# Kernel tuning notes

Measured on AMD Instinct MI355X. Metric: run time of the kernel, lower is better.

The kernel has to match this reference:

```python
import jax, jax.numpy as jnp
import numpy as np

CELL = 128
STEPS = 20
N_KEYS = 4   # ['first_conn','second_conn','first_op','second_op']
N_OUT = 6


def setup_inputs() -> dict:
    key = jax.random.key(0)
    ks = jax.random.split(key, 10)
    s = 0.05
    return {
        "net": jax.random.randint(ks[0], (STEPS,), 0, N_OUT),          # sampled actions, each in [0,6)
        "reward": jax.random.uniform(ks[1], (1,), dtype=jnp.float32),   # unused in forward (kept for signature parity)
        "emb_start": jax.random.normal(ks[2], (1, CELL), jnp.float32) * s,          # Embedding(1,128)
        "emb_keys": jax.random.normal(ks[3], (N_KEYS, N_OUT, CELL), jnp.float32) * s,
        "fc_W": jax.random.normal(ks[4], (N_KEYS, N_OUT, CELL), jnp.float32) * s,
        "fc_b": jax.random.normal(ks[5], (N_KEYS, N_OUT), jnp.float32) * s,
        "W_ih": jax.random.normal(ks[6], (4 * CELL, CELL), jnp.float32) * s,  # LSTMCell input weights (i,f,g,o)
        "W_hh": jax.random.normal(ks[7], (4 * CELL, CELL), jnp.float32) * s,  # LSTMCell hidden weights
        "b_ih": jax.random.normal(ks[8], (4 * CELL,), jnp.float32) * s,
        "b_hh": jax.random.normal(ks[9], (4 * CELL,), jnp.float32) * s,
    }


def _lstm_cell(x, h, c, W_ih, W_hh, b_ih, b_hh):
    # PyTorch LSTMCell: gates ordered (i, f, g, o)
    gates = x @ W_ih.T + b_ih + h @ W_hh.T + b_hh   # [1, 4*CELL]
    i, f, g, o = jnp.split(gates, 4, axis=-1)
    c_new = jax.nn.sigmoid(f) * c + jax.nn.sigmoid(i) * jnp.tanh(g)
    h_new = jax.nn.sigmoid(o) * jnp.tanh(c_new)
    return h_new, c_new


def reference(net, reward, emb_start, emb_keys, fc_W, fc_b, W_ih, W_hh, b_ih, b_hh):
    key_idx = jnp.arange(STEPS) % N_KEYS            # which head/embedding at each step
    fc_W_t = fc_W[key_idx]                          # [STEPS, 6, CELL]
    fc_b_t = fc_b[key_idx]                          # [STEPS, 6]
    emb_t = emb_keys[key_idx, net]                  # [STEPS, CELL] next-step input embedding

    def step(carry, xs):
        h, c, x = carry
        Wt, bt, ev = xs
        h, c = _lstm_cell(x, h, c, W_ih, W_hh, b_ih, b_hh)
        probs = jax.nn.softmax(h @ Wt.T + bt, axis=1)   # [1, 6]
        return (h, c, ev[None, :]), probs

    h0 = jnp.zeros((1, CELL), dtype=emb_start.dtype)
    c0 = jnp.zeros((1, CELL), dtype=emb_start.dtype)
    x0 = emb_start                                   # embedding lookup of action 0 in a 1-row table
    _, outputs = jax.lax.scan(step, (h0, c0, x0), (fc_W_t, fc_b_t, emb_t))
    return outputs                                   # [STEPS, 1, 6], stacked version of the torch list
```

## Files before the change

### kernel.cpp

```cpp
#include <hip/hip_runtime.h>
#include <hip/hip_fp16.h>

#define CELL 128
#define STEPS 20

typedef _Float16 half8_t __attribute__((ext_vector_type(8)));
typedef float    floatx4 __attribute__((ext_vector_type(4)));

__device__ __forceinline__ unsigned packf2(float x, float y) {
    typedef _Float16 h2 __attribute__((ext_vector_type(2)));
    h2 h = { (_Float16)x, (_Float16)y };
    return __builtin_bit_cast(unsigned, h);
}
__device__ __forceinline__ float fdot2u(unsigned a, unsigned b, float c) {
    typedef _Float16 h2 __attribute__((ext_vector_type(2)));
#if __has_builtin(__builtin_amdgcn_fdot2)
    return __builtin_amdgcn_fdot2(__builtin_bit_cast(h2, a), __builtin_bit_cast(h2, b), c, false);
#else
    h2 x = __builtin_bit_cast(h2, a), y = __builtin_bit_cast(h2, b);
    return fmaf((float)x[0], (float)y[0], fmaf((float)x[1], (float)y[1], c));
#endif
}
__device__ __forceinline__ float fast_sigmoid(float x) { return 1.0f / (1.0f + __expf(-x)); }
__device__ __forceinline__ float fast_tanh(float x) {
    return 2.0f / (1.0f + __expf(-2.0f * x)) - 1.0f;
}


__global__ void __launch_bounds__(256)
nas_conv_kernel(const float* __restrict__ W_ih, const float* __restrict__ W_hh,
                const float* __restrict__ b_ih, const float* __restrict__ b_hh,
                uint4* __restrict__ wsf, float* __restrict__ wsb)
{
    const int tid = blockIdx.x * 256 + threadIdx.x;
    for (int f = tid; f < 16384; f += 8192) {
        const int t0 = f >> 5, rem = f & 31, kc = rem >> 2, tau = rem & 3;
        const int wv = t0 >> 6, lane = t0 & 63, quad = lane >> 4, lcol = lane & 15;
        const int r  = (wv << 6) + (tau << 4) + lcol;
        const int k0 = (kc << 5) + (quad << 3);
        const float* src = (k0 < CELL) ? (W_ih + r * CELL + k0)
                                       : (W_hh + r * CELL + (k0 - CELL));
        float4 a = ((const float4*)src)[0], b = ((const float4*)src)[1];
        half8_t h = { (_Float16)a.x, (_Float16)a.y, (_Float16)a.z, (_Float16)a.w,
                      (_Float16)b.x, (_Float16)b.y, (_Float16)b.z, (_Float16)b.w };
        wsf[f] = __builtin_bit_cast(uint4, h);
    }
    if (tid < 512) wsb[tid] = b_ih[tid] + b_hh[tid];
}

extern "C" __global__ void __launch_bounds__(512, 1)
nas_policy_kernel(const int* __restrict__ net,
                  const float* __restrict__ emb_start,
                  const float* __restrict__ emb_keys,
                  const float* __restrict__ fc_W,
                  const float* __restrict__ fc_b,
                  const uint4* __restrict__ wsf,
                  const float* __restrict__ wsb,
                  float* __restrict__ out)
{
    const int t0   = threadIdx.x;
    const int wv   = t0 >> 6;
    const int lane = t0 & 63;
    const int lcol = lane & 15;

    __shared__ __align__(16) unsigned xh2[2 * 64];
    __shared__ __align__(16) unsigned hp2[2 * 64];
    __shared__ __align__(16) unsigned s_embk2[24 * 64];
    __shared__ unsigned s_fcw2[24 * 64];
    __shared__ float gates[4 * CELL];
    __shared__ float s_fcb[24];
    __shared__ float logits[2 * 8];
    __shared__ int   s_net[STEPS];

    const uint4* wf = wsf + t0 * 32;
    half8_t bf0[8], bf1[8], bf2[8], bf3[8];
#pragma unroll
    for (int kc = 0; kc < 8; ++kc) {
        bf0[kc] = __builtin_bit_cast(half8_t, wf[kc * 4 + 0]);
        bf1[kc] = __builtin_bit_cast(half8_t, wf[kc * 4 + 1]);
        bf2[kc] = __builtin_bit_cast(half8_t, wf[kc * 4 + 2]);
        bf3[kc] = __builtin_bit_cast(half8_t, wf[kc * 4 + 3]);
    }
    const int rb = (wv << 6) + lcol;
    const float bias0 = wsb[rb], bias1 = wsb[rb + 16], bias2 = wsb[rb + 32], bias3 = wsb[rb + 48];

    {
        const float2* ek2 = (const float2*)emb_keys;
        const float2* fw2 = (const float2*)fc_W;
        for (int i = t0; i < 24 * 64; i += 512) {
            float2 v = ek2[i]; s_embk2[i] = packf2(v.x, v.y);
            float2 w = fw2[i]; s_fcw2[i]  = packf2(w.x, w.y);
        }
        if (t0 < 24)    s_fcb[t0] = fc_b[t0];
        if (t0 < STEPS) s_net[t0] = net[t0];
        if (t0 < 64) {
            float2 v = ((const float2*)emb_start)[t0];
            xh2[t0]      = packf2(v.x, v.y);
            xh2[64 + t0] = 0u;
        }
    }
    float c = 0.0f;
    const int rbase = wv << 6;

    for (int t = 0; t < STEPS; ++t) {
        __syncthreads();

        floatx4 acc0 = {0,0,0,0}, acc1 = {0,0,0,0}, acc2 = {0,0,0,0}, acc3 = {0,0,0,0};
        const uint4* xp = (const uint4*)xh2;
        const int quad = lane >> 4;
#pragma unroll
        for (int kc = 0; kc < 8; ++kc) {
            uint4 u = xp[(kc << 2) + quad];
            half8_t af = __builtin_bit_cast(half8_t, u);
            acc0 = __builtin_amdgcn_mfma_f32_16x16x32_f16(af, bf0[kc], acc0, 0, 0, 0);
            acc1 = __builtin_amdgcn_mfma_f32_16x16x32_f16(af, bf1[kc], acc1, 0, 0, 0);
            acc2 = __builtin_amdgcn_mfma_f32_16x16x32_f16(af, bf2[kc], acc2, 0, 0, 0);
            acc3 = __builtin_amdgcn_mfma_f32_16x16x32_f16(af, bf3[kc], acc3, 0, 0, 0);
        }
        if (lane < 16) {
            gates[rbase + lane]      = acc0[0] + bias0;
            gates[rbase + 16 + lane] = acc1[0] + bias1;
            gates[rbase + 32 + lane] = acc2[0] + bias2;
            gates[rbase + 48 + lane] = acc3[0] + bias3;
        }

        if (t >= 2 && wv == 5 && lane < 6) {
            const float* L = logits + ((t & 1) << 3);
            float l0 = L[0], l1 = L[1], l2 = L[2], l3 = L[3], l4 = L[4], l5 = L[5];
            float m = fmaxf(fmaxf(fmaxf(l0, l1), fmaxf(l2, l3)), fmaxf(l4, l5));
            float e0 = __expf(l0 - m), e1 = __expf(l1 - m), e2 = __expf(l2 - m);
            float e3 = __expf(l3 - m), e4 = __expf(l4 - m), e5 = __expf(l5 - m);
            float s = ((e0 + e1) + (e2 + e3)) + (e4 + e5);
            float mine = (lane == 0) ? e0 : (lane == 1) ? e1 : (lane == 2) ? e2
                       : (lane == 3) ? e3 : (lane == 4) ? e4 : e5;
            out[(t - 2) * 6 + lane] = mine / s;
        }

        __syncthreads();

        if (t0 < CELL) {
            float ig = fast_sigmoid(gates[t0]);
            float fg = fast_sigmoid(gates[CELL + t0]);
            float gg = fast_tanh   (gates[2 * CELL + t0]);
            float og = fast_sigmoid(gates[3 * CELL + t0]);
            c = fg * c + ig * gg;
            float h = og * fast_tanh(c);
            float hpv = __shfl_xor(h, 1);
            if ((t0 & 1) == 0) {
                unsigned u = packf2(h, hpv);
                xh2[64 + (t0 >> 1)] = u;
                hp2[((t & 1) << 6) + (t0 >> 1)] = u;
            }
        }
        if (wv == 2 && t < STEPS - 1) {
            xh2[lane] = s_embk2[((((t + 1) & 3) * 6) + s_net[t + 1]) * 64 + lane];
        }
        if (t >= 1 && wv >= 2) {
            const int ti = t - 1, hd = wv - 2;
            unsigned hu = hp2[((ti & 1) << 6) + lane];
            unsigned wu = s_fcw2[(((ti & 3) * 6) + hd) * 64 + lane];
            float p = fdot2u(hu, wu, 0.0f);
#pragma unroll
            for (int off = 32; off >= 1; off >>= 1) p += __shfl_down(p, off);
            if (lane == 0)
                logits[((ti & 1) << 3) + hd] = p + s_fcb[(ti & 3) * 6 + hd];
        }
    }

    __syncthreads();
    if (wv >= 2) {
        const int hd = wv - 2;
        unsigned hu = hp2[(1 << 6) + lane];
        unsigned wu = s_fcw2[(((19 & 3) * 6) + hd) * 64 + lane];
        float p = fdot2u(hu, wu, 0.0f);
#pragma unroll
        for (int off = 32; off >= 1; off >>= 1) p += __shfl_down(p, off);
        if (lane == 0) logits[(1 << 3) + hd] = p + s_fcb[(19 & 3) * 6 + hd];
    }
    if (wv == 0 && lane < 6) {
        const float* L = logits + 0;
        float l0 = L[0], l1 = L[1], l2 = L[2], l3 = L[3], l4 = L[4], l5 = L[5];
        float m = fmaxf(fmaxf(fmaxf(l0, l1), fmaxf(l2, l3)), fmaxf(l4, l5));
        float e0 = __expf(l0 - m), e1 = __expf(l1 - m), e2 = __expf(l2 - m);
        float e3 = __expf(l3 - m), e4 = __expf(l4 - m), e5 = __expf(l5 - m);
        float s = ((e0 + e1) + (e2 + e3)) + (e4 + e5);
        float mine = (lane == 0) ? e0 : (lane == 1) ? e1 : (lane == 2) ? e2
                   : (lane == 3) ? e3 : (lane == 4) ? e4 : e5;
        out[18 * 6 + lane] = mine / s;
    }
    __syncthreads();
    if (wv == 0 && lane < 6) {
        const float* L = logits + 8;
        float l0 = L[0], l1 = L[1], l2 = L[2], l3 = L[3], l4 = L[4], l5 = L[5];
        float m = fmaxf(fmaxf(fmaxf(l0, l1), fmaxf(l2, l3)), fmaxf(l4, l5));
        float e0 = __expf(l0 - m), e1 = __expf(l1 - m), e2 = __expf(l2 - m);
        float e3 = __expf(l3 - m), e4 = __expf(l4 - m), e5 = __expf(l5 - m);
        float s = ((e0 + e1) + (e2 + e3)) + (e4 + e5);
        float mine = (lane == 0) ? e0 : (lane == 1) ? e1 : (lane == 2) ? e2
                   : (lane == 3) ? e3 : (lane == 4) ? e4 : e5;
        out[19 * 6 + lane] = mine / s;
    }
}

extern "C" __global__ void __launch_bounds__(512, 1)
nas_policy_fb(const int* __restrict__ net, const float* __restrict__ emb_start,
              const float* __restrict__ emb_keys, const float* __restrict__ fc_W,
              const float* __restrict__ fc_b, const float* __restrict__ W_ih,
              const float* __restrict__ W_hh, const float* __restrict__ b_ih,
              const float* __restrict__ b_hh, float* __restrict__ out)
{
    const int t0 = threadIdx.x, wv = t0 >> 6, lane = t0 & 63;
    const int quad = lane >> 4, lcol = lane & 15;
    __shared__ __align__(16) unsigned xh2[2 * 64];
    __shared__ __align__(16) unsigned s_embk2[24 * 64];
    __shared__ float gates[4 * CELL];
    __shared__ float s_fcW[24 * CELL];
    __shared__ float s_fcb[24];
    __shared__ float logits[2 * 8];
    __shared__ int   s_net[STEPS];
    const int rbase = wv << 6;
    const int r0 = rbase + lcol, r1 = r0 + 16, r2 = r0 + 32, r3 = r0 + 48;
    half8_t bf0[8], bf1[8], bf2[8], bf3[8];
#pragma unroll
    for (int kc = 0; kc < 8; ++kc) {
        const int k0 = (kc << 5) + (quad << 3);
        const float* base = (k0 < 128) ? W_ih + k0 : W_hh + (k0 - 128);
#define LD8(dst, row) { const float4* p4 = (const float4*)(base + (row) * CELL); \
        float4 a = p4[0], b = p4[1]; \
        dst = half8_t{ (_Float16)a.x, (_Float16)a.y, (_Float16)a.z, (_Float16)a.w, \
                       (_Float16)b.x, (_Float16)b.y, (_Float16)b.z, (_Float16)b.w }; }
        LD8(bf0[kc], r0) LD8(bf1[kc], r1) LD8(bf2[kc], r2) LD8(bf3[kc], r3)
#undef LD8
    }
    const float bias0 = b_ih[r0] + b_hh[r0], bias1 = b_ih[r1] + b_hh[r1];
    const float bias2 = b_ih[r2] + b_hh[r2], bias3 = b_ih[r3] + b_hh[r3];
    {
        const float2* ek2 = (const float2*)emb_keys;
        for (int i = t0; i < 24 * 64; i += 512) { float2 v = ek2[i]; s_embk2[i] = packf2(v.x, v.y); }
        for (int i = t0; i < 24 * CELL; i += 512) s_fcW[i] = fc_W[i];
        if (t0 < 24) s_fcb[t0] = fc_b[t0];
        if (t0 < STEPS) s_net[t0] = net[t0];
        if (t0 < 64) { float2 v = ((const float2*)emb_start)[t0];
                       xh2[t0] = packf2(v.x, v.y); xh2[64 + t0] = 0u; }
    }
    float c = 0.0f;
    for (int t = 0; t < STEPS; ++t) {
        __syncthreads();
        floatx4 a0 = {0,0,0,0}, a1 = {0,0,0,0}, a2 = {0,0,0,0}, a3 = {0,0,0,0};
        const uint4* xp = (const uint4*)xh2;
#pragma unroll
        for (int kc = 0; kc < 8; ++kc) {
            half8_t af = __builtin_bit_cast(half8_t, xp[(kc << 2) + quad]);
            a0 = __builtin_amdgcn_mfma_f32_16x16x32_f16(af, bf0[kc], a0, 0, 0, 0);
            a1 = __builtin_amdgcn_mfma_f32_16x16x32_f16(af, bf1[kc], a1, 0, 0, 0);
            a2 = __builtin_amdgcn_mfma_f32_16x16x32_f16(af, bf2[kc], a2, 0, 0, 0);
            a3 = __builtin_amdgcn_mfma_f32_16x16x32_f16(af, bf3[kc], a3, 0, 0, 0);
        }
        if (lane < 16) {
            gates[rbase + lane]      = a0[0] + bias0;
            gates[rbase + 16 + lane] = a1[0] + bias1;
            gates[rbase + 32 + lane] = a2[0] + bias2;
            gates[rbase + 48 + lane] = a3[0] + bias3;
        }
        if (t >= 1 && wv < 6) {
            const int ti = t - 1;
            unsigned hu = xh2[64 + lane];
            const float* Wr = s_fcW + (((ti & 3) * 6) + wv) * CELL;
            typedef _Float16 h2t __attribute__((ext_vector_type(2)));
            h2t hh = __builtin_bit_cast(h2t, hu);
            float p2 = (float)hh[0] * Wr[2 * lane] + (float)hh[1] * Wr[2 * lane + 1];
#pragma unroll
            for (int off = 32; off >= 1; off >>= 1) p2 += __shfl_down(p2, off);
            if (lane == 0) logits[((ti & 1) << 3) + wv] = p2 + s_fcb[(ti & 3) * 6 + wv];
        }
        if (t >= 2 && t0 < 6) {
            const float* L = logits + ((t & 1) << 3);
            float l0 = L[0], l1 = L[1], l2 = L[2], l3 = L[3], l4 = L[4], l5 = L[5];
            float m = fmaxf(fmaxf(fmaxf(l0, l1), fmaxf(l2, l3)), fmaxf(l4, l5));
            float e0 = __expf(l0 - m), e1 = __expf(l1 - m), e2 = __expf(l2 - m);
            float e3 = __expf(l3 - m), e4 = __expf(l4 - m), e5 = __expf(l5 - m);
            float s = ((e0 + e1) + (e2 + e3)) + (e4 + e5);
            float mine = (t0 == 0) ? e0 : (t0 == 1) ? e1 : (t0 == 2) ? e2
                       : (t0 == 3) ? e3 : (t0 == 4) ? e4 : e5;
            out[(t - 2) * 6 + t0] = mine / s;
        }
        __syncthreads();
        if (t0 < CELL) {
            float ig = fast_sigmoid(gates[t0]);
            float fg = fast_sigmoid(gates[CELL + t0]);
            float gg = fast_tanh(gates[2 * CELL + t0]);
            float og = fast_sigmoid(gates[3 * CELL + t0]);
            c = fg * c + ig * gg;
            float h = og * fast_tanh(c);
            float hpv = __shfl_xor(h, 1);
            if ((t0 & 1) == 0) xh2[64 + (t0 >> 1)] = packf2(h, hpv);
        } else if (wv == 2 && t < STEPS - 1) {
            xh2[lane] = s_embk2[((((t + 1) & 3) * 6) + s_net[t + 1]) * 64 + lane];
        }
    }
    __syncthreads();
    if (wv < 6) {
        unsigned hu = xh2[64 + lane];
        const float* Wr = s_fcW + (((19 & 3) * 6) + wv) * CELL;
        typedef _Float16 h2t __attribute__((ext_vector_type(2)));
        h2t hh = __builtin_bit_cast(h2t, hu);
        float p2 = (float)hh[0] * Wr[2 * lane] + (float)hh[1] * Wr[2 * lane + 1];
#pragma unroll
        for (int off = 32; off >= 1; off >>= 1) p2 += __shfl_down(p2, off);
        if (lane == 0) logits[8 + wv] = p2 + s_fcb[(19 & 3) * 6 + wv];
    }
    if (t0 < 6) {
        const float* L = logits + 0;
        float l0 = L[0], l1 = L[1], l2 = L[2], l3 = L[3], l4 = L[4], l5 = L[5];
        float m = fmaxf(fmaxf(fmaxf(l0, l1), fmaxf(l2, l3)), fmaxf(l4, l5));
        float e0 = __expf(l0 - m), e1 = __expf(l1 - m), e2 = __expf(l2 - m);
        float e3 = __expf(l3 - m), e4 = __expf(l4 - m), e5 = __expf(l5 - m);
        float s = ((e0 + e1) + (e2 + e3)) + (e4 + e5);
        float mine = (t0 == 0) ? e0 : (t0 == 1) ? e1 : (t0 == 2) ? e2
                   : (t0 == 3) ? e3 : (t0 == 4) ? e4 : e5;
        out[18 * 6 + t0] = mine / s;
    }
    __syncthreads();
    if (t0 < 6) {
        const float* L = logits + 8;
        float l0 = L[0], l1 = L[1], l2 = L[2], l3 = L[3], l4 = L[4], l5 = L[5];
        float m = fmaxf(fmaxf(fmaxf(l0, l1), fmaxf(l2, l3)), fmaxf(l4, l5));
        float e0 = __expf(l0 - m), e1 = __expf(l1 - m), e2 = __expf(l2 - m);
        float e3 = __expf(l3 - m), e4 = __expf(l4 - m), e5 = __expf(l5 - m);
        float s = ((e0 + e1) + (e2 + e3)) + (e4 + e5);
        float mine = (t0 == 0) ? e0 : (t0 == 1) ? e1 : (t0 == 2) ? e2
                   : (t0 == 3) ? e3 : (t0 == 4) ? e4 : e5;
        out[19 * 6 + t0] = mine / s;
    }
}

extern "C" void kernel_launch(void* const* d_in, const int* in_sizes, int n_in,
                              void* d_out, int out_size, void* d_ws, size_t ws_size,
                              hipStream_t stream) {
    (void)in_sizes; (void)n_in; (void)out_size;
    const int*   net       = (const int*)d_in[0];
    const float* emb_start = (const float*)d_in[2];
    const float* emb_keys  = (const float*)d_in[3];
    const float* fc_W      = (const float*)d_in[4];
    const float* fc_b      = (const float*)d_in[5];
    const float* W_ih      = (const float*)d_in[6];
    const float* W_hh      = (const float*)d_in[7];
    const float* b_ih      = (const float*)d_in[8];
    const float* b_hh      = (const float*)d_in[9];
    float*       out       = (float*)d_out;

    if (ws_size >= (size_t)(262144 + 2048)) {
        uint4* wsf = (uint4*)d_ws;
        float* wsb = (float*)((char*)d_ws + 262144);
        hipLaunchKernelGGL(nas_conv_kernel, dim3(32), dim3(256), 0, stream,
                           W_ih, W_hh, b_ih, b_hh, wsf, wsb);
        hipLaunchKernelGGL(nas_policy_kernel, dim3(1), dim3(512), 0, stream,
                           net, emb_start, emb_keys, fc_W, fc_b, wsf, wsb, out);
    } else {
        hipLaunchKernelGGL(nas_policy_fb, dim3(1), dim3(512), 0, stream,
                           net, emb_start, emb_keys, fc_W, fc_b,
                           W_ih, W_hh, b_ih, b_hh, out);
    }
}
```

Measured before the change: 103.8 us.

## Precompute input-gate projections for all steps and run recurrence on hidden-only MFMAs

The conv kernel now computes W_ih·x + biases for every step up front in fp32. This is possible because the inputs are fixed embeddings chosen by net and do not depend on the recurrence. The policy kernel loads these into shared memory, so each step only needs the W_hh·h MFMAs (half the K). Gate layout is reorganised so each wave's lanes hold the i/f/g/o outputs for the same hidden units directly, removing the gates shared buffer and one barrier per step. Softmax is deferred to a single parallel pass at the end. In exchange it adds a 40KB shared buffer and a heavier pre-kernel, and it changes the fallback kernel's embedding index, which looks like an unrelated bug fix.

```diff
diff --git a/kernel.cpp b/kernel.cpp
--- a/kernel.cpp
+++ b/kernel.cpp
@@ -30,175 +30,150 @@
 __global__ void __launch_bounds__(256)
 nas_conv_kernel(const float* __restrict__ W_ih, const float* __restrict__ W_hh,
                 const float* __restrict__ b_ih, const float* __restrict__ b_hh,
-                uint4* __restrict__ wsf, float* __restrict__ wsb)
+                const float* __restrict__ emb_start, const float* __restrict__ emb_keys,
+                const int* __restrict__ net,
+                uint4* __restrict__ wsf, float* __restrict__ wsg)
 {
     const int tid = blockIdx.x * 256 + threadIdx.x;
-    for (int f = tid; f < 16384; f += 8192) {
-        const int t0 = f >> 5, rem = f & 31, kc = rem >> 2, tau = rem & 3;
+    {
+        const int f = tid;
+        const int t0 = f >> 4, rem = f & 15, kc = rem >> 2, tau = rem & 3;
         const int wv = t0 >> 6, lane = t0 & 63, quad = lane >> 4, lcol = lane & 15;
-        const int r  = (wv << 6) + (tau << 4) + lcol;
-        const int k0 = (kc << 5) + (quad << 3);
-        const float* src = (k0 < CELL) ? (W_ih + r * CELL + k0)
-                                       : (W_hh + r * CELL + (k0 - CELL));
-        float4 a = ((const float4*)src)[0], b = ((const float4*)src)[1];
+        const int r  = tau * 128 + wv * 16 + lcol;
+        const int k0 = kc * 32 + quad * 8;
+        const float4* s4 = (const float4*)(W_hh + r * CELL + k0);
+        float4 a = s4[0], b = s4[1];
         half8_t h = { (_Float16)a.x, (_Float16)a.y, (_Float16)a.z, (_Float16)a.w,
                       (_Float16)b.x, (_Float16)b.y, (_Float16)b.z, (_Float16)b.w };
         wsf[f] = __builtin_bit_cast(uint4, h);
     }
-    if (tid < 512) wsb[tid] = b_ih[tid] + b_hh[tid];
+    for (int f = tid; f < STEPS * 512; f += 8192) {
+        const int t = f >> 9, r = f & 511;
+        const float* x = (t == 0) ? emb_start
+                       : emb_keys + ((((t - 1) & 3) * 6) + net[t - 1]) * CELL;
+        const float4* xr = (const float4*)x;
+        const float4* wr = (const float4*)(W_ih + r * CELL);
+        float a0 = 0.f, a1 = 0.f, a2 = 0.f, a3 = 0.f;
+#pragma unroll
+        for (int q = 0; q < 32; ++q) {
+            float4 w = wr[q], v = xr[q];
+            a0 = fmaf(w.x, v.x, a0); a1 = fmaf(w.y, v.y, a1);
+            a2 = fmaf(w.z, v.z, a2); a3 = fmaf(w.w, v.w, a3);
+        }
+        wsg[f] = (a0 + a1) + (a2 + a3) + b_ih[r] + b_hh[r];
+    }
 }
 
 extern "C" __global__ void __launch_bounds__(512, 1)
-nas_policy_kernel(const int* __restrict__ net,
-                  const float* __restrict__ emb_start,
-                  const float* __restrict__ emb_keys,
-                  const float* __restrict__ fc_W,
+nas_policy_kernel(const float* __restrict__ fc_W,
                   const float* __restrict__ fc_b,
                   const uint4* __restrict__ wsf,
-                  const float* __restrict__ wsb,
+                  const float* __restrict__ wsg,
                   float* __restrict__ out)
 {
     const int t0   = threadIdx.x;
     const int wv   = t0 >> 6;
     const int lane = t0 & 63;
-    const int lcol = lane & 15;
-
-    __shared__ __align__(16) unsigned xh2[2 * 64];
-    __shared__ __align__(16) unsigned hp2[2 * 64];
-    __shared__ __align__(16) unsigned s_embk2[24 * 64];
+    const int quad = lane >> 4;
+
+    __shared__ __align__(16) unsigned hbuf[2 * 64];
+    __shared__ __align__(16) float    s_gx[STEPS * 512];
     __shared__ unsigned s_fcw2[24 * 64];
-    __shared__ float gates[4 * CELL];
-    __shared__ float s_fcb[24];
-    __shared__ float logits[2 * 8];
-    __shared__ int   s_net[STEPS];
-
-    const uint4* wf = wsf + t0 * 32;
-    half8_t bf0[8], bf1[8], bf2[8], bf3[8];
-#pragma unroll
-    for (int kc = 0; kc < 8; ++kc) {
+    __shared__ float    s_fcb[24];
+    __shared__ float    llog[STEPS * 8];
+
+    const uint4* wf = wsf + t0 * 16;
+    half8_t bf0[4], bf1[4], bf2[4], bf3[4];
+#pragma unroll
+    for (int kc = 0; kc < 4; ++kc) {
         bf0[kc] = __builtin_bit_cast(half8_t, wf[kc * 4 + 0]);
         bf1[kc] = __builtin_bit_cast(half8_t, wf[kc * 4 + 1]);
         bf2[kc] = __builtin_bit_cast(half8_t, wf[kc * 4 + 2]);
         bf3[kc] = __builtin_bit_cast(half8_t, wf[kc * 4 + 3]);
     }
-    const int rb = (wv << 6) + lcol;
-    const float bias0 = wsb[rb], bias1 = wsb[rb + 16], bias2 = wsb[rb + 32], bias3 = wsb[rb + 48];
 
     {
-        const float2* ek2 = (const float2*)emb_keys;
+        const float4* g4 = (const float4*)wsg;
+        float4* sg4 = (float4*)s_gx;
+        for (int i = t0; i < STEPS * 128; i += 512) sg4[i] = g4[i];
         const float2* fw2 = (const float2*)fc_W;
-        for (int i = t0; i < 24 * 64; i += 512) {
-            float2 v = ek2[i]; s_embk2[i] = packf2(v.x, v.y);
-            float2 w = fw2[i]; s_fcw2[i]  = packf2(w.x, w.y);
-        }
-        if (t0 < 24)    s_fcb[t0] = fc_b[t0];
-        if (t0 < STEPS) s_net[t0] = net[t0];
-        if (t0 < 64) {
-            float2 v = ((const float2*)emb_start)[t0];
-            xh2[t0]      = packf2(v.x, v.y);
-            xh2[64 + t0] = 0u;
-        }
+        for (int i = t0; i < 24 * 64; i += 512) { float2 w = fw2[i]; s_fcw2[i] = packf2(w.x, w.y); }
+        if (t0 < 24) s_fcb[t0] = fc_b[t0];
+        if (t0 < 64) hbuf[64 + t0] = 0u;
     }
     float c = 0.0f;
-    const int rbase = wv << 6;
+    __syncthreads();
 
     for (int t = 0; t < STEPS; ++t) {
-        __syncthreads();
-
-        floatx4 acc0 = {0,0,0,0}, acc1 = {0,0,0,0}, acc2 = {0,0,0,0}, acc3 = {0,0,0,0};
-        const uint4* xp = (const uint4*)xh2;
-        const int quad = lane >> 4;
-#pragma unroll
-        for (int kc = 0; kc < 8; ++kc) {
-            uint4 u = xp[(kc << 2) + quad];
+        const uint4* hp4 = (const uint4*)(hbuf + (((t + 1) & 1) << 6));
+        floatx4 a0 = {0,0,0,0}, a1 = {0,0,0,0}, a2 = {0,0,0,0}, a3 = {0,0,0,0};
+#pragma unroll
+        for (int kc = 0; kc < 4; ++kc) {
+            uint4 u = hp4[(kc << 2) + quad];
             half8_t af = __builtin_bit_cast(half8_t, u);
-            acc0 = __builtin_amdgcn_mfma_f32_16x16x32_f16(af, bf0[kc], acc0, 0, 0, 0);
-            acc1 = __builtin_amdgcn_mfma_f32_16x16x32_f16(af, bf1[kc], acc1, 0, 0, 0);
-            acc2 = __builtin_amdgcn_mfma_f32_16x16x32_f16(af, bf2[kc], acc2, 0, 0, 0);
-            acc3 = __builtin_amdgcn_mfma_f32_16x16x32_f16(af, bf3[kc], acc3, 0, 0, 0);
-        }
+            a0 = __builtin_amdgcn_mfma_f32_16x16x32_f16(af, bf0[kc], a0, 0, 0, 0);
+            a1 = __builtin_amdgcn_mfma_f32_16x16x32_f16(af, bf1[kc], a1, 0, 0, 0);
+            a2 = __builtin_amdgcn_mfma_f32_16x16x32_f16(af, bf2[kc], a2, 0, 0, 0);
+            a3 = __builtin_amdgcn_mfma_f32_16x16x32_f16(af, bf3[kc], a3, 0, 0, 0);
+        }
+
+        if (t >= 1 && wv >= 6 && lane >= 16) {
+            const int hd = (wv - 6) * 3 + (lane >> 4) - 1;
+            const int li = lane & 15;
+            const int hg = ((t - 1) & 3) * 6 + hd;
+            const unsigned* hb = hbuf + (((t + 1) & 1) << 6);
+            const unsigned* wp = s_fcw2 + hg * 64 + li * 4;
+            float p = fdot2u(hb[li * 4],     wp[0], 0.0f);
+            p = fdot2u(hb[li * 4 + 1], wp[1], p);
+            p = fdot2u(hb[li * 4 + 2], wp[2], p);
+            p = fdot2u(hb[li * 4 + 3], wp[3], p);
+            p += __shfl_down(p, 8); p += __shfl_down(p, 4);
+            p += __shfl_down(p, 2); p += __shfl_down(p, 1);
+            if (li == 0) llog[(t - 1) * 8 + hd] = p + s_fcb[hg];
+        }
+
         if (lane < 16) {
-            gates[rbase + lane]      = acc0[0] + bias0;
-            gates[rbase + 16 + lane] = acc1[0] + bias1;
-            gates[rbase + 32 + lane] = acc2[0] + bias2;
-            gates[rbase + 48 + lane] = acc3[0] + bias3;
-        }
-
-        if (t >= 2 && wv == 5 && lane < 6) {
-            const float* L = logits + ((t & 1) << 3);
-            float l0 = L[0], l1 = L[1], l2 = L[2], l3 = L[3], l4 = L[4], l5 = L[5];
-            float m = fmaxf(fmaxf(fmaxf(l0, l1), fmaxf(l2, l3)), fmaxf(l4, l5));
-            float e0 = __expf(l0 - m), e1 = __expf(l1 - m), e2 = __expf(l2 - m);
-            float e3 = __expf(l3 - m), e4 = __expf(l4 - m), e5 = __expf(l5 - m);
-            float s = ((e0 + e1) + (e2 + e3)) + (e4 + e5);
-            float mine = (lane == 0) ? e0 : (lane == 1) ? e1 : (lane == 2) ? e2
-                       : (lane == 3) ? e3 : (lane == 4) ? e4 : e5;
-            out[(t - 2) * 6 + lane] = mine / s;
-        }
-
-        __syncthreads();
-
-        if (t0 < CELL) {
-            float ig = fast_sigmoid(gates[t0]);
-            float fg = fast_sigmoid(gates[CELL + t0]);
-            float gg = fast_tanh   (gates[2 * CELL + t0]);
-            float og = fast_sigmoid(gates[3 * CELL + t0]);
+            const int base = t * 512 + (wv << 4) + lane;
+            float ig = fast_sigmoid(a0[0] + s_gx[base]);
+            float fg = fast_sigmoid(a1[0] + s_gx[base + 128]);
+            float gg = fast_tanh   (a2[0] + s_gx[base + 256]);
+            float og = fast_sigmoid(a3[0] + s_gx[base + 384]);
             c = fg * c + ig * gg;
             float h = og * fast_tanh(c);
             float hpv = __shfl_xor(h, 1);
-            if ((t0 & 1) == 0) {
-                unsigned u = packf2(h, hpv);
-                xh2[64 + (t0 >> 1)] = u;
-                hp2[((t & 1) << 6) + (t0 >> 1)] = u;
-            }
-        }
-        if (wv == 2 && t < STEPS - 1) {
-            xh2[lane] = s_embk2[((((t + 1) & 3) * 6) + s_net[t + 1]) * 64 + lane];
-        }
-        if (t >= 1 && wv >= 2) {
-            const int ti = t - 1, hd = wv - 2;
-            unsigned hu = hp2[((ti & 1) << 6) + lane];
-            unsigned wu = s_fcw2[(((ti & 3) * 6) + hd) * 64 + lane];
-            float p = fdot2u(hu, wu, 0.0f);
-#pragma unroll
-            for (int off = 32; off >= 1; off >>= 1) p += __shfl_down(p, off);
-            if (lane == 0)
-                logits[((ti & 1) << 3) + hd] = p + s_fcb[(ti & 3) * 6 + hd];
-        }
-    }
-
+            if ((lane & 1) == 0)
+                hbuf[((t & 1) << 6) + (wv << 3) + (lane >> 1)] = packf2(h, hpv);
+        }
+
+        __syncthreads();
+    }
+
+    if (wv >= 6 && lane >= 16) {
+        const int hd = (wv - 6) * 3 + (lane >> 4) - 1;
+        const int li = lane & 15;
+        const int hg = (19 & 3) * 6 + hd;
+        const unsigned* hb = hbuf + 64;
+        const unsigned* wp = s_fcw2 + hg * 64 + li * 4;
+        float p = fdot2u(hb[li * 4],     wp[0], 0.0f);
+        p = fdot2u(hb[li * 4 + 1], wp[1], p);
+        p = fdot2u(hb[li * 4 + 2], wp[2], p);
+        p = fdot2u(hb[li * 4 + 3], wp[3], p);
+        p += __shfl_down(p, 8); p += __shfl_down(p, 4);
+        p += __shfl_down(p, 2); p += __shfl_down(p, 1);
+        if (li == 0) llog[19 * 8 + hd] = p + s_fcb[hg];
+    }
     __syncthreads();
-    if (wv >= 2) {
-        const int hd = wv - 2;
-        unsigned hu = hp2[(1 << 6) + lane];
-        unsigned wu = s_fcw2[(((19 & 3) * 6) + hd) * 64 + lane];
-        float p = fdot2u(hu, wu, 0.0f);
-#pragma unroll
-        for (int off = 32; off >= 1; off >>= 1) p += __shfl_down(p, off);
-        if (lane == 0) logits[(1 << 3) + hd] = p + s_fcb[(19 & 3) * 6 + hd];
-    }
-    if (wv == 0 && lane < 6) {
-        const float* L = logits + 0;
+    if (t0 < STEPS * 6) {
+        const int s = t0 / 6, k = t0 - s * 6;
+        const float* L = llog + s * 8;
         float l0 = L[0], l1 = L[1], l2 = L[2], l3 = L[3], l4 = L[4], l5 = L[5];
         float m = fmaxf(fmaxf(fmaxf(l0, l1), fmaxf(l2, l3)), fmaxf(l4, l5));
         float e0 = __expf(l0 - m), e1 = __expf(l1 - m), e2 = __expf(l2 - m);
         float e3 = __expf(l3 - m), e4 = __expf(l4 - m), e5 = __expf(l5 - m);
-        float s = ((e0 + e1) + (e2 + e3)) + (e4 + e5);
-        float mine = (lane == 0) ? e0 : (lane == 1) ? e1 : (lane == 2) ? e2
-                   : (lane == 3) ? e3 : (lane == 4) ? e4 : e5;
-        out[18 * 6 + lane] = mine / s;
-    }
-    __syncthreads();
-    if (wv == 0 && lane < 6) {
-        const float* L = logits + 8;
-        float l0 = L[0], l1 = L[1], l2 = L[2], l3 = L[3], l4 = L[4], l5 = L[5];
-        float m = fmaxf(fmaxf(fmaxf(l0, l1), fmaxf(l2, l3)), fmaxf(l4, l5));
-        float e0 = __expf(l0 - m), e1 = __expf(l1 - m), e2 = __expf(l2 - m);
-        float e3 = __expf(l3 - m), e4 = __expf(l4 - m), e5 = __expf(l5 - m);
-        float s = ((e0 + e1) + (e2 + e3)) + (e4 + e5);
-        float mine = (lane == 0) ? e0 : (lane == 1) ? e1 : (lane == 2) ? e2
-                   : (lane == 3) ? e3 : (lane == 4) ? e4 : e5;
-        out[19 * 6 + lane] = mine / s;
+        float sum = ((e0 + e1) + (e2 + e3)) + (e4 + e5);
+        float mine = (k == 0) ? e0 : (k == 1) ? e1 : (k == 2) ? e2
+                   : (k == 3) ? e3 : (k == 4) ? e4 : e5;
+        out[t0] = mine / sum;
     }
 }
 
@@ -279,10 +254,10 @@
             float m = fmaxf(fmaxf(fmaxf(l0, l1), fmaxf(l2, l3)), fmaxf(l4, l5));
             float e0 = __expf(l0 - m), e1 = __expf(l1 - m), e2 = __expf(l2 - m);
             float e3 = __expf(l3 - m), e4 = __expf(l4 - m), e5 = __expf(l5 - m);
-            float s = ((e0 + e1) + (e2 + e3)) + (e4 + e5);
+            float ssum = ((e0 + e1) + (e2 + e3)) + (e4 + e5);
             float mine = (t0 == 0) ? e0 : (t0 == 1) ? e1 : (t0 == 2) ? e2
                        : (t0 == 3) ? e3 : (t0 == 4) ? e4 : e5;
-            out[(t - 2) * 6 + t0] = mine / s;
+            out[(t - 2) * 6 + t0] = mine / ssum;
         }
         __syncthreads();
         if (t0 < CELL) {
@@ -295,7 +270,7 @@
             float hpv = __shfl_xor(h, 1);
             if ((t0 & 1) == 0) xh2[64 + (t0 >> 1)] = packf2(h, hpv);
         } else if (wv == 2 && t < STEPS - 1) {
-            xh2[lane] = s_embk2[((((t + 1) & 3) * 6) + s_net[t + 1]) * 64 + lane];
+            xh2[lane] = s_embk2[(((t & 3) * 6) + s_net[t]) * 64 + lane];
         }
     }
     __syncthreads();
@@ -315,10 +290,10 @@
         float m = fmaxf(fmaxf(fmaxf(l0, l1), fmaxf(l2, l3)), fmaxf(l4, l5));
         float e0 = __expf(l0 - m), e1 = __expf(l1 - m), e2 = __expf(l2 - m);
         float e3 = __expf(l3 - m), e4 = __expf(l4 - m), e5 = __expf(l5 - m);
-        float s = ((e0 + e1) + (e2 + e3)) + (e4 + e5);
+        float ssum = ((e0 + e1) + (e2 + e3)) + (e4 + e5);
         float mine = (t0 == 0) ? e0 : (t0 == 1) ? e1 : (t0 == 2) ? e2
                    : (t0 == 3) ? e3 : (t0 == 4) ? e4 : e5;
-        out[18 * 6 + t0] = mine / s;
+        out[18 * 6 + t0] = mine / ssum;
     }
     __syncthreads();
     if (t0 < 6) {
@@ -327,10 +302,10 @@
         float m = fmaxf(fmaxf(fmaxf(l0, l1), fmaxf(l2, l3)), fmaxf(l4, l5));
         float e0 = __expf(l0 - m), e1 = __expf(l1 - m), e2 = __expf(l2 - m);
         float e3 = __expf(l3 - m), e4 = __expf(l4 - m), e5 = __expf(l5 - m);
-        float s = ((e0 + e1) + (e2 + e3)) + (e4 + e5);
+        float ssum = ((e0 + e1) + (e2 + e3)) + (e4 + e5);
         float mine = (t0 == 0) ? e0 : (t0 == 1) ? e1 : (t0 == 2) ? e2
                    : (t0 == 3) ? e3 : (t0 == 4) ? e4 : e5;
-        out[19 * 6 + t0] = mine / s;
+        out[19 * 6 + t0] = mine / ssum;
     }
 }
 
@@ -349,13 +324,13 @@
     const float* b_hh      = (const float*)d_in[9];
     float*       out       = (float*)d_out;
 
-    if (ws_size >= (size_t)(262144 + 2048)) {
+    if (ws_size >= (size_t)(131072 + STEPS * 512 * sizeof(float))) {
         uint4* wsf = (uint4*)d_ws;
-        float* wsb = (float*)((char*)d_ws + 262144);
+        float* wsg = (float*)((char*)d_ws + 131072);
         hipLaunchKernelGGL(nas_conv_kernel, dim3(32), dim3(256), 0, stream,
-                           W_ih, W_hh, b_ih, b_hh, wsf, wsb);
+                           W_ih, W_hh, b_ih, b_hh, emb_start, emb_keys, net, wsf, wsg);
         hipLaunchKernelGGL(nas_policy_kernel, dim3(1), dim3(512), 0, stream,
-                           net, emb_start, emb_keys, fc_W, fc_b, wsf, wsb, out);
+                           fc_W, fc_b, wsf, wsg, out);
     } else {
         hipLaunchKernelGGL(nas_policy_fb, dim3(1), dim3(512), 0, stream,
                            net, emb_start, emb_keys, fc_W, fc_b,
```

Result: slower. 105.9 us (+2.0%).
